# Kernel tuning notes

Hardware: AMD Instinct MI355X
Metric: run time of the kernel (lower is better)

The kernel has to match this reference:

```python
import jax, jax.numpy as jnp
import numpy as np

N, M, D = 4096, 4096, 8

def laplace_tensor_markov(x, grid, lengthscale):
    # product over dims of exp(-|x_i - y_j|/ls) == exp(-sum_d |x_id - y_jd|/ls_d)
    # x: [n,d], grid: [m,d] -> [n,m]
    diff = jnp.abs(x[:, None, :] - grid[None, :, :]) / lengthscale  # [n,m,d]
    return jnp.exp(-jnp.sum(diff, axis=-1))

def setup_inputs() -> dict:
    key = jax.random.key(0)
    k1, k2, k3 = jax.random.split(key, 3)
    x = jax.random.normal(k1, (N, D), dtype=jnp.float32)
    sparse_grid = jax.random.uniform(k2, (M, D), dtype=jnp.float32)
    # inverse Cholesky factor is lower-triangular; emulate its structured sparsity
    L = jax.random.normal(k3, (M, M), dtype=jnp.float32) * 0.02
    chol_inv = jnp.tril(L) + jnp.eye(M, dtype=jnp.float32)
    lengthscale = jnp.ones((D,), dtype=jnp.float32)
    return {"x": x, "sparse_grid": sparse_grid, "chol_inv": chol_inv, "lengthscale": lengthscale}

def reference(x, sparse_grid, chol_inv, lengthscale):
    k_star = laplace_tensor_markov(x, sparse_grid, lengthscale)  # [n,m]
    phi = k_star @ chol_inv                                      # [n,m]
    return phi
```

## Files before the change

kernel.cpp:

```cpp
#include <hip/hip_runtime.h>
#include <cstdint>
#include <cstddef>

typedef unsigned short u16;
typedef __bf16 bf16x8 __attribute__((ext_vector_type(8)));
typedef float floatx4 __attribute__((ext_vector_type(4)));

#define NPTS 4096
#define MGRD 4096
#define DDIM 8

static __device__ __forceinline__ u16 f2bf(float f) {
    uint32_t u = __float_as_uint(f);
    u += 0x7fffu + ((u >> 16) & 1u);
    return (u16)(u >> 16);
}

__global__ __launch_bounds__(256) void prep_kernel(
    const float* __restrict__ x, const float* __restrict__ g,
    const float* __restrict__ ls, const float* __restrict__ B,
    u16* __restrict__ A, u16* __restrict__ Bt)
{
    __shared__ float tile[64][65];
    const int bid = blockIdx.x;
    const int tid = threadIdx.x;

    if (bid < 512) {
        const int kb = bid & 1;
        const int n0 = (bid >> 1) * 16;
        const int k0 = kb * 2048 + tid * 8;

        float il[DDIM];
#pragma unroll
        for (int d = 0; d < DDIM; ++d) il[d] = 1.0f / ls[d];

        float4 g0[8], g1[8];
#pragma unroll
        for (int r = 0; r < 8; ++r) {
            g0[r] = *reinterpret_cast<const float4*>(g + (size_t)(k0 + r) * DDIM);
            g1[r] = *reinterpret_cast<const float4*>(g + (size_t)(k0 + r) * DDIM + 4);
        }

        for (int nn = 0; nn < 16; ++nn) {
            const int n = n0 + nn;
            const float4 x0 = *reinterpret_cast<const float4*>(x + (size_t)n * DDIM);
            const float4 x1 = *reinterpret_cast<const float4*>(x + (size_t)n * DDIM + 4);
            alignas(16) u16 res[8];
#pragma unroll
            for (int r = 0; r < 8; ++r) {
                float s = fabsf(x0.x - g0[r].x) * il[0] + fabsf(x0.y - g0[r].y) * il[1]
                        + fabsf(x0.z - g0[r].z) * il[2] + fabsf(x0.w - g0[r].w) * il[3]
                        + fabsf(x1.x - g1[r].x) * il[4] + fabsf(x1.y - g1[r].y) * il[5]
                        + fabsf(x1.z - g1[r].z) * il[6] + fabsf(x1.w - g1[r].w) * il[7];
                res[r] = f2bf(__expf(-s));
            }
            *reinterpret_cast<uint4*>(A + (size_t)n * MGRD + k0) =
                *reinterpret_cast<const uint4*>(res);
        }
    } else {
        const int id = bid - 512;
        const int bx = id & 63;
        const int by = id >> 6;
        if (by < (bx & ~1)) return;
        const int k0 = by * 64;
        const int m0 = bx * 64;

#pragma unroll
        for (int r = 0; r < 4; ++r) {
            int c   = r * 256 + tid;
            int row = c >> 4;
            int col = (c & 15) * 4;
            const float4 v = *reinterpret_cast<const float4*>(&B[(size_t)(k0 + row) * MGRD + m0 + col]);
            tile[row][col + 0] = v.x; tile[row][col + 1] = v.y;
            tile[row][col + 2] = v.z; tile[row][col + 3] = v.w;
        }
        __syncthreads();

#pragma unroll
        for (int r = 0; r < 2; ++r) {
            int c  = r * 256 + tid;
            int mr = c >> 3;
            int kc = (c & 7) * 8;
            alignas(16) u16 tmp[8];
#pragma unroll
            for (int j = 0; j < 8; ++j)
                tmp[j] = f2bf(tile[kc + j][mr]);
            *reinterpret_cast<uint4*>(&Bt[(size_t)(m0 + mr) * MGRD + k0 + kc]) =
                *reinterpret_cast<const uint4*>(tmp);
        }
    }
}


#define FENCE() asm volatile("" ::: "memory")
static __device__ __forceinline__ void bar() {
    FENCE(); __builtin_amdgcn_s_barrier(); FENCE();
}

__global__ __launch_bounds__(512, 2) void gemm_sb_kernel(
    const u16* __restrict__ A,
    const u16* __restrict__ Bt,
    float* __restrict__ C)
{
    __shared__ u16 lds[3 * 24576] __attribute__((aligned(16)));

    const int tid  = threadIdx.x;
    const int lane = tid & 63;
    const int w    = tid >> 6;
    const int kg   = w >> 2;
    const int wq   = w & 3;
    const int nq   = wq >> 1;
    const int mq   = wq & 1;
    const int lrow = lane & 15;
    const int lhi  = lane >> 4;
    const int r7   = lrow & 7;

    const int id  = blockIdx.x;
    const int bm  = id >> 4;
    const int bn  = id & 15;
    const int bn0 = bn << 8;
    const int bm0 = bm << 7;
    const int L   = 64 - 2 * bm;

    const int arow = tid >> 3;
    const int aswz = ((tid ^ arow) & 7) * 8;
    int aoff[4], boff[2];
#pragma unroll
    for (int r = 0; r < 4; ++r)
        aoff[r] = (bn0 + r * 64 + arow) * 4096 + aswz;
#pragma unroll
    for (int r = 0; r < 2; ++r)
        boff[r] = (bm0 + r * 64 + arow) * 4096 + aswz;

    const int ldst = w * 512;
    const int cswz = ((kg * 4 + lhi) ^ r7) * 8;
    const int rowA = (nq * 128 + lrow) * 64 + cswz;
    const int rowB = (mq * 64  + lrow) * 64 + cswz;

#define STG_A(QA, R, K) __builtin_amdgcn_global_load_lds(                        \
    (const __attribute__((address_space(1))) void*)(A + (size_t)aoff[R] + (K)),  \
    (__attribute__((address_space(3))) void*)((QA) + (R) * 4096 + ldst), 16, 0, 0)
#define STG_B(QB, R, K) __builtin_amdgcn_global_load_lds(                        \
    (const __attribute__((address_space(1))) void*)(Bt + (size_t)boff[R] + (K)), \
    (__attribute__((address_space(3))) void*)((QB) + (R) * 4096 + ldst), 16, 0, 0)

    bf16x8 af[8], bfv[4];

#define RDALL(PA, PB) do {                                                       \
    af[0]  = *reinterpret_cast<const bf16x8*>((PA) + rowA + 0 * 1024);           \
    bfv[0] = *reinterpret_cast<const bf16x8*>((PB) + rowB + 0 * 1024);           \
    bfv[1] = *reinterpret_cast<const bf16x8*>((PB) + rowB + 1 * 1024);           \
    bfv[2] = *reinterpret_cast<const bf16x8*>((PB) + rowB + 2 * 1024);           \
    bfv[3] = *reinterpret_cast<const bf16x8*>((PB) + rowB + 3 * 1024);           \
    af[1]  = *reinterpret_cast<const bf16x8*>((PA) + rowA + 1 * 1024);           \
    af[2]  = *reinterpret_cast<const bf16x8*>((PA) + rowA + 2 * 1024);           \
    af[3]  = *reinterpret_cast<const bf16x8*>((PA) + rowA + 3 * 1024);           \
    af[4]  = *reinterpret_cast<const bf16x8*>((PA) + rowA + 4 * 1024);           \
    af[5]  = *reinterpret_cast<const bf16x8*>((PA) + rowA + 5 * 1024);           \
    af[6]  = *reinterpret_cast<const bf16x8*>((PA) + rowA + 6 * 1024);           \
    af[7]  = *reinterpret_cast<const bf16x8*>((PA) + rowA + 7 * 1024);           \
} while (0)

    floatx4 acc[8][4];
#pragma unroll
    for (int i = 0; i < 8; ++i)
#pragma unroll
        for (int j = 0; j < 4; ++j)
            acc[i][j] = (floatx4)0.0f;

#define MF(a, b, c) __builtin_amdgcn_mfma_f32_16x16x32_bf16(a, b, c, 0, 0, 0)
#define MFMA32() do {                                                            \
    __builtin_amdgcn_s_setprio(1);                                               \
    _Pragma("unroll")                                                            \
    for (int i_ = 0; i_ < 8; ++i_)                                               \
        _Pragma("unroll")                                                        \
        for (int j_ = 0; j_ < 4; ++j_)                                           \
            acc[i_][j_] = MF(af[i_], bfv[j_], acc[i_][j_]);                      \
    __builtin_amdgcn_s_setprio(0);                                               \
} while (0)

    int kT = 4096 - 64;
    {
        u16* qA0 = lds;                 u16* qB0 = lds + 16384;
        u16* qA1 = lds + 24576;         u16* qB1 = lds + 24576 + 16384;
        STG_A(qA0, 0, kT); STG_A(qA0, 1, kT); STG_A(qA0, 2, kT); STG_A(qA0, 3, kT);
        STG_B(qB0, 0, kT); STG_B(qB0, 1, kT);
        STG_A(qA1, 0, kT - 64); STG_A(qA1, 1, kT - 64);
        STG_A(qA1, 2, kT - 64); STG_A(qA1, 3, kT - 64);
        STG_B(qB1, 0, kT - 64); STG_B(qB1, 1, kT - 64);
    }
    asm volatile("s_waitcnt vmcnt(6)" ::: "memory");
    bar();

    int p = 0;
    for (int T = 0; T < L - 2; ++T) {
        u16* pA = lds + p * 24576;      u16* pB = pA + 16384;
        int p2 = p + 2; if (p2 >= 3) p2 -= 3;
        u16* qA = lds + p2 * 24576;     u16* qB = qA + 16384;
        const int kst = kT - 128;

        STG_A(qA, 0, kst); STG_A(qA, 1, kst); STG_A(qA, 2, kst); STG_A(qA, 3, kst);
        STG_B(qB, 0, kst); STG_B(qB, 1, kst);
        RDALL(pA, pB);
        MFMA32();
        asm volatile("s_waitcnt vmcnt(6)" ::: "memory");
        bar();

        kT -= 64; ++p; if (p == 3) p = 0;
    }

    {
        u16* pA = lds + p * 24576;      u16* pB = pA + 16384;
        RDALL(pA, pB);
        MFMA32();
        asm volatile("s_waitcnt vmcnt(0)" ::: "memory");
        bar();
        ++p; if (p == 3) p = 0;
    }
    {
        u16* pA = lds + p * 24576;      u16* pB = pA + 16384;
        RDALL(pA, pB);
        MFMA32();
    }

    __syncthreads();
    float* scr = reinterpret_cast<float*>(lds);
    if (kg == 1) {
#pragma unroll
        for (int i = 0; i < 8; ++i)
#pragma unroll
            for (int j = 0; j < 4; ++j)
                *reinterpret_cast<floatx4*>(
                    scr + (size_t)wq * 8192 + (i * 4 + j) * 256 + lane * 4) = acc[i][j];
    }
    __syncthreads();
    if (kg == 0) {
#pragma unroll
        for (int i = 0; i < 8; ++i)
#pragma unroll
            for (int j = 0; j < 4; ++j)
                acc[i][j] += *reinterpret_cast<const floatx4*>(
                    scr + (size_t)wq * 8192 + (i * 4 + j) * 256 + lane * 4);

#pragma unroll
        for (int i = 0; i < 8; ++i) {
            int rown = bn0 + nq * 128 + i * 16 + lhi * 4;
#pragma unroll
            for (int j = 0; j < 4; ++j) {
                int colm = bm0 + mq * 64 + j * 16 + lrow;
                float* cp = C + (size_t)rown * 4096 + colm;
#pragma unroll
                for (int rr = 0; rr < 4; ++rr)
                    cp[(size_t)rr * 4096] = acc[i][j][rr];
            }
        }
    }
}

extern "C" void kernel_launch(void* const* d_in, const int* in_sizes, int n_in,
                              void* d_out, int out_size, void* d_ws, size_t ws_size,
                              hipStream_t stream)
{
    const float* x    = (const float*)d_in[0];
    const float* grid = (const float*)d_in[1];
    const float* ci   = (const float*)d_in[2];
    const float* ls   = (const float*)d_in[3];
    float* out = (float*)d_out;

    u16* wsA  = (u16*)d_ws;
    u16* wsBt = (u16*)d_ws + (size_t)MGRD * MGRD;

    prep_kernel<<<dim3(512 + 64 * 64), 256, 0, stream>>>(x, grid, ls, ci, wsA, wsBt);
    gemm_sb_kernel<<<dim3(512), 512, 0, stream>>>(wsA, wsBt, out);
}
```

Baseline: 185.1 us.

## Double-buffer MFMA register fragments to overlap LDS reads with matrix math

Splits the A/B fragment registers into two sets and unrolls the K loop by two, so the LDS reads for the next tile are issued before the MFMAs for the current tile. This hides LDS read latency behind matrix instructions. In exchange each iteration now needs two barriers instead of one, and the extra fragment registers raise register pressure, which may hurt the two-blocks-per-CU occupancy target. The loop also assumes L-2 is even.

```diff
diff --git a/kernel.cpp b/kernel.cpp
--- a/kernel.cpp
+++ b/kernel.cpp
@@ -97,7 +97,7 @@
     FENCE(); __builtin_amdgcn_s_barrier(); FENCE();
 }
 
-__global__ __launch_bounds__(512, 2) void gemm_sb_kernel(
+__global__ __launch_bounds__(512, 2) void gemm_rdb_kernel(
     const u16* __restrict__ A,
     const u16* __restrict__ Bt,
     float* __restrict__ C)
@@ -143,22 +143,26 @@
 #define STG_B(QB, R, K) __builtin_amdgcn_global_load_lds(                        \
     (const __attribute__((address_space(1))) void*)(Bt + (size_t)boff[R] + (K)), \
     (__attribute__((address_space(3))) void*)((QB) + (R) * 4096 + ldst), 16, 0, 0)
-
-    bf16x8 af[8], bfv[4];
-
-#define RDALL(PA, PB) do {                                                       \
-    af[0]  = *reinterpret_cast<const bf16x8*>((PA) + rowA + 0 * 1024);           \
-    bfv[0] = *reinterpret_cast<const bf16x8*>((PB) + rowB + 0 * 1024);           \
-    bfv[1] = *reinterpret_cast<const bf16x8*>((PB) + rowB + 1 * 1024);           \
-    bfv[2] = *reinterpret_cast<const bf16x8*>((PB) + rowB + 2 * 1024);           \
-    bfv[3] = *reinterpret_cast<const bf16x8*>((PB) + rowB + 3 * 1024);           \
-    af[1]  = *reinterpret_cast<const bf16x8*>((PA) + rowA + 1 * 1024);           \
-    af[2]  = *reinterpret_cast<const bf16x8*>((PA) + rowA + 2 * 1024);           \
-    af[3]  = *reinterpret_cast<const bf16x8*>((PA) + rowA + 3 * 1024);           \
-    af[4]  = *reinterpret_cast<const bf16x8*>((PA) + rowA + 4 * 1024);           \
-    af[5]  = *reinterpret_cast<const bf16x8*>((PA) + rowA + 5 * 1024);           \
-    af[6]  = *reinterpret_cast<const bf16x8*>((PA) + rowA + 6 * 1024);           \
-    af[7]  = *reinterpret_cast<const bf16x8*>((PA) + rowA + 7 * 1024);           \
+#define STG6(QA, QB, K) do {                                                     \
+    STG_A(QA, 0, K); STG_A(QA, 1, K); STG_A(QA, 2, K); STG_A(QA, 3, K);          \
+    STG_B(QB, 0, K); STG_B(QB, 1, K);                                            \
+} while (0)
+
+    bf16x8 af0[8], bv0[4], af1[8], bv1[4];
+
+#define RDALL(AF, BV, PA, PB) do {                                               \
+    AF[0] = *reinterpret_cast<const bf16x8*>((PA) + rowA + 0 * 1024);            \
+    BV[0] = *reinterpret_cast<const bf16x8*>((PB) + rowB + 0 * 1024);            \
+    BV[1] = *reinterpret_cast<const bf16x8*>((PB) + rowB + 1 * 1024);            \
+    BV[2] = *reinterpret_cast<const bf16x8*>((PB) + rowB + 2 * 1024);            \
+    BV[3] = *reinterpret_cast<const bf16x8*>((PB) + rowB + 3 * 1024);            \
+    AF[1] = *reinterpret_cast<const bf16x8*>((PA) + rowA + 1 * 1024);            \
+    AF[2] = *reinterpret_cast<const bf16x8*>((PA) + rowA + 2 * 1024);            \
+    AF[3] = *reinterpret_cast<const bf16x8*>((PA) + rowA + 3 * 1024);            \
+    AF[4] = *reinterpret_cast<const bf16x8*>((PA) + rowA + 4 * 1024);            \
+    AF[5] = *reinterpret_cast<const bf16x8*>((PA) + rowA + 5 * 1024);            \
+    AF[6] = *reinterpret_cast<const bf16x8*>((PA) + rowA + 6 * 1024);            \
+    AF[7] = *reinterpret_cast<const bf16x8*>((PA) + rowA + 7 * 1024);            \
 } while (0)
 
     floatx4 acc[8][4];
@@ -169,13 +173,13 @@
             acc[i][j] = (floatx4)0.0f;
 
 #define MF(a, b, c) __builtin_amdgcn_mfma_f32_16x16x32_bf16(a, b, c, 0, 0, 0)
-#define MFMA32() do {                                                            \
+#define MFMA32(AF, BV) do {                                                      \
     __builtin_amdgcn_s_setprio(1);                                               \
     _Pragma("unroll")                                                            \
     for (int i_ = 0; i_ < 8; ++i_)                                               \
         _Pragma("unroll")                                                        \
         for (int j_ = 0; j_ < 4; ++j_)                                           \
-            acc[i_][j_] = MF(af[i_], bfv[j_], acc[i_][j_]);                      \
+            acc[i_][j_] = MF(AF[i_], BV[j_], acc[i_][j_]);                       \
     __builtin_amdgcn_s_setprio(0);                                               \
 } while (0)
 
@@ -183,44 +187,53 @@
     {
         u16* qA0 = lds;                 u16* qB0 = lds + 16384;
         u16* qA1 = lds + 24576;         u16* qB1 = lds + 24576 + 16384;
-        STG_A(qA0, 0, kT); STG_A(qA0, 1, kT); STG_A(qA0, 2, kT); STG_A(qA0, 3, kT);
-        STG_B(qB0, 0, kT); STG_B(qB0, 1, kT);
-        STG_A(qA1, 0, kT - 64); STG_A(qA1, 1, kT - 64);
-        STG_A(qA1, 2, kT - 64); STG_A(qA1, 3, kT - 64);
-        STG_B(qB1, 0, kT - 64); STG_B(qB1, 1, kT - 64);
+        STG6(qA0, qB0, kT);
+        STG6(qA1, qB1, kT - 64);
     }
     asm volatile("s_waitcnt vmcnt(6)" ::: "memory");
     bar();
+    RDALL(af0, bv0, lds, lds + 16384);
 
     int p = 0;
-    for (int T = 0; T < L - 2; ++T) {
-        u16* pA = lds + p * 24576;      u16* pB = pA + 16384;
+    for (int T = 0; T < L - 2; T += 2) {
+        int p1 = p + 1; if (p1 >= 3) p1 -= 3;
         int p2 = p + 2; if (p2 >= 3) p2 -= 3;
-        u16* qA = lds + p2 * 24576;     u16* qB = qA + 16384;
-        const int kst = kT - 128;
-
-        STG_A(qA, 0, kst); STG_A(qA, 1, kst); STG_A(qA, 2, kst); STG_A(qA, 3, kst);
-        STG_B(qB, 0, kst); STG_B(qB, 1, kst);
-        RDALL(pA, pB);
-        MFMA32();
-        asm volatile("s_waitcnt vmcnt(6)" ::: "memory");
-        bar();
-
-        kT -= 64; ++p; if (p == 3) p = 0;
+
+        {
+            u16* qA = lds + p2 * 24576;  u16* qB = qA + 16384;
+            STG6(qA, qB, kT - 128);
+            asm volatile("s_waitcnt vmcnt(6)" ::: "memory");
+            bar();
+            u16* rA = lds + p1 * 24576;  u16* rB = rA + 16384;
+            RDALL(af1, bv1, rA, rB);
+            MFMA32(af0, bv0);
+            bar();
+        }
+        kT -= 64;
+
+        {
+            u16* qA = lds + p * 24576;   u16* qB = qA + 16384;
+            STG6(qA, qB, kT - 128);
+            asm volatile("s_waitcnt vmcnt(6)" ::: "memory");
+            bar();
+            u16* rA = lds + p2 * 24576;  u16* rB = rA + 16384;
+            RDALL(af0, bv0, rA, rB);
+            MFMA32(af1, bv1);
+            bar();
+        }
+        kT -= 64;
+
+        p += 2; if (p >= 3) p -= 3;
     }
 
     {
-        u16* pA = lds + p * 24576;      u16* pB = pA + 16384;
-        RDALL(pA, pB);
-        MFMA32();
+        int p1 = p + 1; if (p1 >= 3) p1 -= 3;
         asm volatile("s_waitcnt vmcnt(0)" ::: "memory");
         bar();
-        ++p; if (p == 3) p = 0;
-    }
-    {
-        u16* pA = lds + p * 24576;      u16* pB = pA + 16384;
-        RDALL(pA, pB);
-        MFMA32();
+        u16* rA = lds + p1 * 24576;  u16* rB = rA + 16384;
+        RDALL(af1, bv1, rA, rB);
+        MFMA32(af0, bv0);
+        MFMA32(af1, bv1);
     }
 
     __syncthreads();
@@ -271,5 +284,5 @@
     u16* wsBt = (u16*)d_ws + (size_t)MGRD * MGRD;
 
     prep_kernel<<<dim3(512 + 64 * 64), 256, 0, stream>>>(x, grid, ls, ci, wsA, wsBt);
-    gemm_sb_kernel<<<dim3(512), 512, 0, stream>>>(wsA, wsBt, out);
-}
+    gemm_rdb_kernel<<<dim3(512), 512, 0, stream>>>(wsA, wsBt, out);
+}
```

After: 194.5 us. 1.05x slower.

## Pair triangular tiles per block to balance work and interleave staging loads

Applied to the files above, without the earlier changes.

Each block now handles two output column tiles, bm and 31-bm, so every block does the same total K-iteration count across the triangular chol_inv structure. The grid halves to 256 blocks, one per CU. The main loop also interleaves the async global-to-LDS stage loads with the LDS fragment reads to spread memory issue. The risk is that the prologue and epilogue of the two tiles run back to back without overlap, and there is less occupancy slack for hiding latency.

```diff
diff --git a/kernel.cpp b/kernel.cpp
--- a/kernel.cpp
+++ b/kernel.cpp
@@ -97,7 +97,7 @@
     FENCE(); __builtin_amdgcn_s_barrier(); FENCE();
 }
 
-__global__ __launch_bounds__(512, 2) void gemm_sb_kernel(
+__global__ __launch_bounds__(512, 2) void gemm_pair_kernel(
     const u16* __restrict__ A,
     const u16* __restrict__ Bt,
     float* __restrict__ C)
@@ -116,21 +116,16 @@
     const int r7   = lrow & 7;
 
     const int id  = blockIdx.x;
-    const int bm  = id >> 4;
+    const int bm1 = id >> 4;
     const int bn  = id & 15;
     const int bn0 = bn << 8;
-    const int bm0 = bm << 7;
-    const int L   = 64 - 2 * bm;
 
     const int arow = tid >> 3;
     const int aswz = ((tid ^ arow) & 7) * 8;
-    int aoff[4], boff[2];
+    int aoff[4];
 #pragma unroll
     for (int r = 0; r < 4; ++r)
         aoff[r] = (bn0 + r * 64 + arow) * 4096 + aswz;
-#pragma unroll
-    for (int r = 0; r < 2; ++r)
-        boff[r] = (bm0 + r * 64 + arow) * 4096 + aswz;
 
     const int ldst = w * 512;
     const int cswz = ((kg * 4 + lhi) ^ r7) * 8;
@@ -145,6 +140,38 @@
     (__attribute__((address_space(3))) void*)((QB) + (R) * 4096 + ldst), 16, 0, 0)
 
     bf16x8 af[8], bfv[4];
+
+    floatx4 acc[8][4];
+
+#define MF(a, b, c) __builtin_amdgcn_mfma_f32_16x16x32_bf16(a, b, c, 0, 0, 0)
+#define MFMA32() do {                                                            \
+    __builtin_amdgcn_s_setprio(1);                                               \
+    _Pragma("unroll")                                                            \
+    for (int i_ = 0; i_ < 8; ++i_)                                               \
+        _Pragma("unroll")                                                        \
+        for (int j_ = 0; j_ < 4; ++j_)                                           \
+            acc[i_][j_] = MF(af[i_], bfv[j_], acc[i_][j_]);                      \
+    __builtin_amdgcn_s_setprio(0);                                               \
+} while (0)
+
+#define REGION(PA, PB, QA, QB, KST) do {                                         \
+    STG_A(QA, 0, KST); STG_A(QA, 1, KST);                                        \
+    af[0]  = *reinterpret_cast<const bf16x8*>((PA) + rowA + 0 * 1024);           \
+    bfv[0] = *reinterpret_cast<const bf16x8*>((PB) + rowB + 0 * 1024);           \
+    bfv[1] = *reinterpret_cast<const bf16x8*>((PB) + rowB + 1 * 1024);           \
+    bfv[2] = *reinterpret_cast<const bf16x8*>((PB) + rowB + 2 * 1024);           \
+    bfv[3] = *reinterpret_cast<const bf16x8*>((PB) + rowB + 3 * 1024);           \
+    STG_A(QA, 2, KST); STG_A(QA, 3, KST);                                        \
+    af[1]  = *reinterpret_cast<const bf16x8*>((PA) + rowA + 1 * 1024);           \
+    af[2]  = *reinterpret_cast<const bf16x8*>((PA) + rowA + 2 * 1024);           \
+    af[3]  = *reinterpret_cast<const bf16x8*>((PA) + rowA + 3 * 1024);           \
+    STG_B(QB, 0, KST); STG_B(QB, 1, KST);                                        \
+    af[4]  = *reinterpret_cast<const bf16x8*>((PA) + rowA + 4 * 1024);           \
+    af[5]  = *reinterpret_cast<const bf16x8*>((PA) + rowA + 5 * 1024);           \
+    af[6]  = *reinterpret_cast<const bf16x8*>((PA) + rowA + 6 * 1024);           \
+    af[7]  = *reinterpret_cast<const bf16x8*>((PA) + rowA + 7 * 1024);           \
+    MFMA32();                                                                    \
+} while (0)
 
 #define RDALL(PA, PB) do {                                                       \
     af[0]  = *reinterpret_cast<const bf16x8*>((PA) + rowA + 0 * 1024);           \
@@ -161,99 +188,95 @@
     af[7]  = *reinterpret_cast<const bf16x8*>((PA) + rowA + 7 * 1024);           \
 } while (0)
 
-    floatx4 acc[8][4];
-#pragma unroll
-    for (int i = 0; i < 8; ++i)
-#pragma unroll
-        for (int j = 0; j < 4; ++j)
-            acc[i][j] = (floatx4)0.0f;
-
-#define MF(a, b, c) __builtin_amdgcn_mfma_f32_16x16x32_bf16(a, b, c, 0, 0, 0)
-#define MFMA32() do {                                                            \
-    __builtin_amdgcn_s_setprio(1);                                               \
-    _Pragma("unroll")                                                            \
-    for (int i_ = 0; i_ < 8; ++i_)                                               \
-        _Pragma("unroll")                                                        \
-        for (int j_ = 0; j_ < 4; ++j_)                                           \
-            acc[i_][j_] = MF(af[i_], bfv[j_], acc[i_][j_]);                      \
-    __builtin_amdgcn_s_setprio(0);                                               \
-} while (0)
-
-    int kT = 4096 - 64;
-    {
-        u16* qA0 = lds;                 u16* qB0 = lds + 16384;
-        u16* qA1 = lds + 24576;         u16* qB1 = lds + 24576 + 16384;
-        STG_A(qA0, 0, kT); STG_A(qA0, 1, kT); STG_A(qA0, 2, kT); STG_A(qA0, 3, kT);
-        STG_B(qB0, 0, kT); STG_B(qB0, 1, kT);
-        STG_A(qA1, 0, kT - 64); STG_A(qA1, 1, kT - 64);
-        STG_A(qA1, 2, kT - 64); STG_A(qA1, 3, kT - 64);
-        STG_B(qB1, 0, kT - 64); STG_B(qB1, 1, kT - 64);
-    }
-    asm volatile("s_waitcnt vmcnt(6)" ::: "memory");
-    bar();
-
-    int p = 0;
-    for (int T = 0; T < L - 2; ++T) {
-        u16* pA = lds + p * 24576;      u16* pB = pA + 16384;
-        int p2 = p + 2; if (p2 >= 3) p2 -= 3;
-        u16* qA = lds + p2 * 24576;     u16* qB = qA + 16384;
-        const int kst = kT - 128;
-
-        STG_A(qA, 0, kst); STG_A(qA, 1, kst); STG_A(qA, 2, kst); STG_A(qA, 3, kst);
-        STG_B(qB, 0, kst); STG_B(qB, 1, kst);
-        RDALL(pA, pB);
-        MFMA32();
+    for (int jj = 0; jj < 2; ++jj) {
+        const int bm  = jj ? (31 - bm1) : bm1;
+        const int bm0 = bm << 7;
+        const int L   = 64 - 2 * bm;
+
+        int boff[2];
+#pragma unroll
+        for (int r = 0; r < 2; ++r)
+            boff[r] = (bm0 + r * 64 + arow) * 4096 + aswz;
+
+#pragma unroll
+        for (int i = 0; i < 8; ++i)
+#pragma unroll
+            for (int j = 0; j < 4; ++j)
+                acc[i][j] = (floatx4)0.0f;
+
+        int kT = 4096 - 64;
+        {
+            u16* qA0 = lds;             u16* qB0 = lds + 16384;
+            u16* qA1 = lds + 24576;     u16* qB1 = lds + 24576 + 16384;
+            STG_A(qA0, 0, kT); STG_A(qA0, 1, kT); STG_A(qA0, 2, kT); STG_A(qA0, 3, kT);
+            STG_B(qB0, 0, kT); STG_B(qB0, 1, kT);
+            STG_A(qA1, 0, kT - 64); STG_A(qA1, 1, kT - 64);
+            STG_A(qA1, 2, kT - 64); STG_A(qA1, 3, kT - 64);
+            STG_B(qB1, 0, kT - 64); STG_B(qB1, 1, kT - 64);
+        }
         asm volatile("s_waitcnt vmcnt(6)" ::: "memory");
         bar();
 
-        kT -= 64; ++p; if (p == 3) p = 0;
-    }
-
-    {
-        u16* pA = lds + p * 24576;      u16* pB = pA + 16384;
-        RDALL(pA, pB);
-        MFMA32();
-        asm volatile("s_waitcnt vmcnt(0)" ::: "memory");
-        bar();
-        ++p; if (p == 3) p = 0;
-    }
-    {
-        u16* pA = lds + p * 24576;      u16* pB = pA + 16384;
-        RDALL(pA, pB);
-        MFMA32();
-    }
-
-    __syncthreads();
-    float* scr = reinterpret_cast<float*>(lds);
-    if (kg == 1) {
-#pragma unroll
-        for (int i = 0; i < 8; ++i)
-#pragma unroll
-            for (int j = 0; j < 4; ++j)
-                *reinterpret_cast<floatx4*>(
-                    scr + (size_t)wq * 8192 + (i * 4 + j) * 256 + lane * 4) = acc[i][j];
-    }
-    __syncthreads();
-    if (kg == 0) {
-#pragma unroll
-        for (int i = 0; i < 8; ++i)
-#pragma unroll
-            for (int j = 0; j < 4; ++j)
-                acc[i][j] += *reinterpret_cast<const floatx4*>(
-                    scr + (size_t)wq * 8192 + (i * 4 + j) * 256 + lane * 4);
-
-#pragma unroll
-        for (int i = 0; i < 8; ++i) {
-            int rown = bn0 + nq * 128 + i * 16 + lhi * 4;
-#pragma unroll
-            for (int j = 0; j < 4; ++j) {
-                int colm = bm0 + mq * 64 + j * 16 + lrow;
-                float* cp = C + (size_t)rown * 4096 + colm;
-#pragma unroll
-                for (int rr = 0; rr < 4; ++rr)
-                    cp[(size_t)rr * 4096] = acc[i][j][rr];
+        int p = 0;
+        for (int T = 0; T < L - 2; ++T) {
+            u16* pA = lds + p * 24576;  u16* pB = pA + 16384;
+            int p2 = p + 2; if (p2 >= 3) p2 -= 3;
+            u16* qA = lds + p2 * 24576; u16* qB = qA + 16384;
+
+            REGION(pA, pB, qA, qB, kT - 128);
+            asm volatile("s_waitcnt vmcnt(6)" ::: "memory");
+            bar();
+
+            kT -= 64; ++p; if (p == 3) p = 0;
+        }
+
+        {
+            u16* pA = lds + p * 24576;  u16* pB = pA + 16384;
+            RDALL(pA, pB);
+            MFMA32();
+            asm volatile("s_waitcnt vmcnt(0)" ::: "memory");
+            bar();
+            ++p; if (p == 3) p = 0;
+        }
+        {
+            u16* pA = lds + p * 24576;  u16* pB = pA + 16384;
+            RDALL(pA, pB);
+            MFMA32();
+        }
+
+        __syncthreads();
+        float* scr = reinterpret_cast<float*>(lds);
+        if (kg == 1) {
+#pragma unroll
+            for (int i = 0; i < 8; ++i)
+#pragma unroll
+                for (int j = 0; j < 4; ++j)
+                    *reinterpret_cast<floatx4*>(
+                        scr + (size_t)wq * 8192 + (i * 4 + j) * 256 + lane * 4) = acc[i][j];
+        }
+        __syncthreads();
+        if (kg == 0) {
+#pragma unroll
+            for (int i = 0; i < 8; ++i)
+#pragma unroll
+                for (int j = 0; j < 4; ++j)
+                    acc[i][j] += *reinterpret_cast<const floatx4*>(
+                        scr + (size_t)wq * 8192 + (i * 4 + j) * 256 + lane * 4);
+
+#pragma unroll
+            for (int i = 0; i < 8; ++i) {
+                int rown = bn0 + nq * 128 + i * 16 + lhi * 4;
+#pragma unroll
+                for (int j = 0; j < 4; ++j) {
+                    int colm = bm0 + mq * 64 + j * 16 + lrow;
+                    float* cp = C + (size_t)rown * 4096 + colm;
+#pragma unroll
+                    for (int rr = 0; rr < 4; ++rr)
+                        cp[(size_t)rr * 4096] = acc[i][j][rr];
+                }
             }
         }
+        __syncthreads();
     }
 }
 
@@ -271,5 +294,5 @@
     u16* wsBt = (u16*)d_ws + (size_t)MGRD * MGRD;
 
     prep_kernel<<<dim3(512 + 64 * 64), 256, 0, stream>>>(x, grid, ls, ci, wsA, wsBt);
-    gemm_sb_kernel<<<dim3(512), 512, 0, stream>>>(wsA, wsBt, out);
-}
+    gemm_pair_kernel<<<dim3(256), 512, 0, stream>>>(wsA, wsBt, out);
+}
```

Result: no change. 185.1 us (median of 2 runs) (-0.0%).
